# Kernel optimization log

Hardware: AMD Instinct MI355X
Metric: run time of the kernel (lower is better)

Reference implementation:

```python
import jax, jax.numpy as jnp
import numpy as np

PS = 16          # patch size == conv kernel == stride
EPS = 1e-5       # BatchNorm eps (torch default)


def setup_inputs() -> dict:
    key = jax.random.key(0)
    ks = jax.random.split(key, 12)
    B, Cin, H = 64, 3, 256
    D, Dm = 3, 768                      # private_depth, hidden_dim
    P = (H // PS) ** 2                  # num_patches = 256

    x = jax.random.normal(ks[0], (B, Cin, H, H), jnp.float32)
    # patch-embed conv: weight [O, I, kh, kw], bias [O]
    conv0_w = jax.random.normal(ks[1], (Dm, Cin, PS, PS), jnp.float32) * 0.02
    conv0_b = jax.random.normal(ks[2], (Dm,), jnp.float32) * 0.02
    # depth x (1x1 conv + BN): stacked params
    w1 = jax.random.normal(ks[3], (D, Dm, Dm), jnp.float32) * 0.02   # [O, I]
    b1 = jax.random.normal(ks[4], (D, Dm), jnp.float32) * 0.02
    gamma = jnp.ones((D, Dm), jnp.float32)
    beta = jnp.zeros((D, Dm), jnp.float32)
    # positional embedding [1, P, Dm]
    pos_emb = jax.random.normal(ks[5], (1, P, Dm), jnp.float32)
    # mixer Linear [out, in] + bias
    mixer_w = jax.random.normal(ks[6], (Dm, Dm), jnp.float32) * 0.02
    mixer_b = jax.random.normal(ks[7], (Dm,), jnp.float32) * 0.02
    # per-sample random permutation of the P patches (replaces randperm loop)
    perm = jax.vmap(lambda k: jax.random.permutation(k, P))(
        jax.random.split(ks[8], B)).astype(jnp.int32)

    return {"x": x, "conv0_w": conv0_w, "conv0_b": conv0_b, "w1": w1,
            "b1": b1, "gamma": gamma, "beta": beta, "pos_emb": pos_emb,
            "mixer_w": mixer_w, "mixer_b": mixer_b, "perm": perm}


def reference(x, conv0_w, conv0_b, w1, b1, gamma, beta, pos_emb,
              mixer_w, mixer_b, perm):
    B, Cin, H, W = x.shape
    hp, wp = H // PS, W // PS
    Dm = conv0_w.shape[0]

    # non-overlapping patch conv == reshape + matmul
    # x -> [B, hp*wp, Cin*PS*PS] with (c, kh, kw) flattening matching conv weight
    patches = x.reshape(B, Cin, hp, PS, wp, PS).transpose(0, 2, 4, 1, 3, 5)
    patches = patches.reshape(B, hp * wp, Cin * PS * PS)
    h = jax.nn.relu(patches @ conv0_w.reshape(Dm, -1).T + conv0_b)  # [B, P, Dm]

    # private_depth x (1x1 conv -> BN (batch stats, no running stats) -> ReLU)
    for d in range(w1.shape[0]):
        h = h @ w1[d].T + b1[d]
        mu = h.mean(axis=(0, 1))                      # per-channel over (B, H*W)
        var = ((h - mu) ** 2).mean(axis=(0, 1))       # biased variance
        h = (h - mu) * jax.lax.rsqrt(var + EPS) * gamma[d] + beta[d]
        h = jax.nn.relu(h)

    # pos embedding + mixer (ReLU -> Linear)
    h = h + pos_emb
    h = jax.nn.relu(h) @ mixer_w.T + mixer_b          # [B, P, Dm]

    # per-sample pixel shuffle: shuffled[i, j] = h[i, perm[i, j]]
    out = jnp.take_along_axis(h, perm[:, :, None].astype(jnp.int32), axis=1)
    return out
```

## Files before the change

kernel.cpp:

```cpp
#include <hip/hip_runtime.h>
#include <hip/hip_bf16.h>
#include <stdint.h>

#define M_TOT 16384
#define DM 768
#define BM 256
#define BN 192
#define NKT3 12
#define QOFF (128 * DM)

typedef __attribute__((ext_vector_type(4))) float f32x4;
typedef __attribute__((ext_vector_type(8))) short short8;
typedef __attribute__((ext_vector_type(8))) unsigned short ushort8;
typedef __attribute__((ext_vector_type(4))) unsigned short ushort4v;

__device__ __forceinline__ unsigned short f2bf(float f) {
    union { float f; unsigned u; } v; v.f = f;
    unsigned r = v.u + 0x7fffu + ((v.u >> 16) & 1u);
    return (unsigned short)(r >> 16);
}
__device__ __forceinline__ float bf2f(unsigned short h) {
    union { unsigned u; float f; } v; v.u = ((unsigned)h) << 16;
    return v.f;
}

__device__ __forceinline__ void gload_lds16(const unsigned short* g, unsigned short* l) {
    __builtin_amdgcn_global_load_lds(
        (const __attribute__((address_space(1))) void*)g,
        (__attribute__((address_space(3))) void*)l, 16, 0, 0);
}

__global__ __launch_bounds__(256)
void prep(const float* __restrict__ cw, const float* __restrict__ w1,
          const float* __restrict__ mw, const int* __restrict__ perm,
          unsigned short* __restrict__ wA, unsigned short* __restrict__ wD,
          unsigned short* __restrict__ wM, int* __restrict__ invp)
{
    int b = blockIdx.x;
    if (b < 2880) {
        int i = b * 256 + threadIdx.x;
        const float* src; unsigned short* dst; int off;
        if (i < 147456)              { src = cw; dst = wA; off = i; }
        else if (i < 147456+442368)  { src = w1; dst = wD; off = i - 147456; }
        else                         { src = mw; dst = wM; off = i - 589824; }
        f32x4 v = ((const f32x4*)src)[off];
        ushort4v o;
        o.x = f2bf(v.x); o.y = f2bf(v.y); o.z = f2bf(v.z); o.w = f2bf(v.w);
        ((ushort4v*)dst)[off] = o;
    } else {
        int i = (b - 2880) * 256 + threadIdx.x;
        int bb = i >> 8;
        invp[(bb << 8) + perm[i]] = i & 255;
    }
}

__global__ __launch_bounds__(256)
void im2col(const float* __restrict__ x, unsigned short* __restrict__ patches)
{
    int t = blockIdx.x * 256 + threadIdx.x;
    int bp = t / 192;
    int q  = t - bp * 192;
    int c   = q >> 6;
    int kh  = (q >> 2) & 15;
    int kw0 = (q & 3) << 2;
    int b = bp >> 8, p = bp & 255;
    int ph = p >> 4, pw = p & 15;
    const float* src = x + ((((size_t)b * 3 + c) * 256 + ph * 16 + kh) * 256 + pw * 16 + kw0);
    f32x4 v = *(const f32x4*)src;
    ushort4v o;
    o.x = f2bf(v.x); o.y = f2bf(v.y); o.z = f2bf(v.z); o.w = f2bf(v.w);
    *(ushort4v*)(patches + (size_t)bp * DM + (q << 2)) = o;
}

#define VM4  asm volatile("s_waitcnt vmcnt(4)" ::: "memory");
#define VM0  asm volatile("s_waitcnt vmcnt(0)" ::: "memory");
#define LGKM0 asm volatile("s_waitcnt lgkmcnt(0)" ::: "memory");
#define BARR asm volatile("s_barrier" ::: "memory");

#define PH(AB, BB, MH, KS, LOADB, PRE, POST)                                     \
  {                                                                              \
    if (LOADB) {                                                                 \
      _Pragma("unroll")                                                          \
      for (int j = 0; j < 3; ++j)                                                \
        breg[j] = *(const short8*)((const char*)Bb + (size_t)(BB) * (BN*64*2) +  \
                  (wc * 48 + j * 16 + frow) * 128 + (((KS) * 64 + fq16) ^ rswz));\
    }                                                                            \
    short8 af[4];                                                                \
    _Pragma("unroll")                                                            \
    for (int i = 0; i < 4; ++i)                                                  \
      af[i] = *(const short8*)((const char*)Aa + (size_t)(AB) * (BM*64*2) +      \
              (wr * 128 + (MH) * 64 + i * 16 + frow) * 128 +                     \
              (((KS) * 64 + fq16) ^ rswz));                                      \
    PRE;                                                                         \
    __builtin_amdgcn_s_setprio(1);                                               \
    _Pragma("unroll")                                                            \
    for (int i = 0; i < 4; ++i)                                                  \
      _Pragma("unroll")                                                          \
      for (int j = 0; j < 3; ++j)                                                \
        acc[(MH) * 4 + i][j] = __builtin_amdgcn_mfma_f32_16x16x32_bf16(          \
            af[i], breg[j], acc[(MH) * 4 + i][j], 0, 0, 0);                      \
    __builtin_amdgcn_s_setprio(0);                                               \
    POST;                                                                        \
    BARR                                                                         \
  }

template<int EPI, int BNA>
__global__ __launch_bounds__(512, 2)
void gemm8p(const unsigned short* __restrict__ A,
            const unsigned short* __restrict__ Bw,
            const float* __restrict__ bias,
            void* __restrict__ outp,
            const int* __restrict__ invp,
            float* __restrict__ bnpart,
            const float* __restrict__ ssA,
            const float* __restrict__ pos)
{
    __shared__ unsigned short Aa[3][BM * 64];
    __shared__ unsigned short Bb[2][BN * 64];

    const int tid  = threadIdx.x;
    const int w    = tid >> 6;
    const int lane = tid & 63;
    const int wr = w >> 2, wc = w & 3;

    int bid = blockIdx.x;
    int nb  = (bid & 7) * 32 + (bid >> 3);
    const int tileM = nb >> 2, tileN = nb & 3;
    const int m0 = tileM * BM, n0 = tileN * BN;

    const int sRow = lane >> 3;
    const int swzc = ((lane & 7) * 16) ^ ((sRow & 7) << 4);
    const unsigned short* gA0 = A  + (size_t)(m0 + w * 32 + sRow) * DM + (swzc >> 1);
    const unsigned short* gB0 = Bw + (size_t)(n0 + w * 24 + sRow) * DM + (swzc >> 1);

    auto STAGE_A = [&](int buf, int kt) {
        #pragma unroll
        for (int j = 0; j < 4; ++j)
            gload_lds16(gA0 + (size_t)j * 8 * DM + kt * 64,
                        &Aa[buf][(w * 32 + j * 8) * 64]);
    };
    auto STAGE_B = [&](int buf, int kt) {
        #pragma unroll
        for (int j = 0; j < 3; ++j)
            gload_lds16(gB0 + (size_t)j * 8 * DM + kt * 64,
                        &Bb[buf][(w * 24 + j * 8) * 64]);
    };

    const int rRow0 = w * 32 + (lane >> 3);
    const unsigned short* gAr = A + (size_t)(m0 + rRow0) * DM + (lane & 7) * 8;
    const int wrswz = (lane >> 3) << 4;
    ushort8 aldr[4];

    auto ALOAD = [&](int t) {
        #pragma unroll
        for (int j = 0; j < 4; ++j)
            aldr[j] = *(const ushort8*)(gAr + (size_t)j * 8 * DM + t * 64);
    };
    auto XFORM = [&](int t, int tb) {
        const int k0 = t * 64 + (lane & 7) * 8;
        f32x4 sa = *(const f32x4*)(ssA + k0);
        f32x4 sb = *(const f32x4*)(ssA + k0 + 4);
        f32x4 ha = *(const f32x4*)(ssA + DM + k0);
        f32x4 hb = *(const f32x4*)(ssA + DM + k0 + 4);
        #pragma unroll
        for (int j = 0; j < 4; ++j) {
            int row = rRow0 + j * 8;
            f32x4 pa, pb;
            if (BNA == 2) {
                pa = *(const f32x4*)(pos + row * DM + k0);
                pb = *(const f32x4*)(pos + row * DM + k0 + 4);
            }
            ushort8 u = aldr[j];
            ushort8 o;
            #pragma unroll
            for (int e = 0; e < 8; ++e) {
                float f = bf2f(u[e]);
                float sc = (e < 4) ? sa[e] : sb[e - 4];
                float sh = (e < 4) ? ha[e] : hb[e - 4];
                float y = fmaxf(fmaf(sc, f, sh), 0.0f);
                if (BNA == 2) {
                    float pv = (e < 4) ? pa[e] : pb[e - 4];
                    y = fmaxf(y + pv, 0.0f);
                }
                o[e] = f2bf(y);
            }
            *(ushort8*)((char*)Aa + (size_t)tb * (BM*64*2) + row * 128 +
                        (((lane & 7) * 16) ^ wrswz)) = o;
        }
    };

    const int frow = lane & 15;
    const int fq16 = (lane >> 4) * 16;
    const int rswz = (lane & 7) << 4;

    f32x4 acc[8][3] = {};
    short8 breg[3];

    if (BNA == 0) {
        STAGE_A(0, 0);
        STAGE_B(0, 0);
        STAGE_A(1, 1);
        VM4
        BARR
    } else {
        ALOAD(0); XFORM(0, 0);
        ALOAD(1); XFORM(1, 1);
        STAGE_B(0, 0);
        VM0
        LGKM0
        BARR
    }

    if (BNA == 0) {
        #pragma unroll
        for (int kt = 0; kt < NKT3; ++kt) {
            const int ab = kt % 3, bb = kt & 1;
            PH(ab, bb, 0, 0, 1, { if (kt < 11) STAGE_B((kt + 1) & 1, kt + 1); }, {})
            PH(ab, bb, 1, 0, 0, { if (kt < 10) STAGE_A((kt + 2) % 3, kt + 2); }, {})
            PH(ab, bb, 0, 1, 1, {}, {})
            if (kt < 10)       { PH(ab, bb, 1, 1, 0, {}, { VM4 }) }
            else if (kt == 10) { PH(ab, bb, 1, 1, 0, {}, { VM0 }) }
            else               { PH(ab, bb, 1, 1, 0, {}, {}) }
        }
    } else {
        #pragma unroll 3
        for (int kt = 0; kt < NKT3; ++kt) {
            const int ab = kt % 3, bb = kt & 1;
            const int ab1 = (ab == 2) ? 0 : ab + 1;
            PH(ab, bb, 0, 0, 1, { if (kt < 11) STAGE_B((kt + 1) & 1, kt + 1); }, {})
            PH(ab, bb, 1, 0, 0, { if (kt >= 1 && kt < 11) XFORM(kt + 1, ab1); },
                                { if (kt >= 1 && kt < 11) LGKM0 })
            PH(ab, bb, 0, 1, 1, {}, {})
            PH(ab, bb, 1, 1, 0, {}, { if (kt < 11) VM0
                                      if (kt < 10) ALOAD(kt + 2); })
        }
    }

    const int crow = (lane >> 4) * 4;
    const int ccol = lane & 15;
    const int nbase = n0 + wc * 48;

    float bv[3];
    #pragma unroll
    for (int j = 0; j < 3; ++j) bv[j] = bias[nbase + j * 16 + ccol];

    if (EPI == 0) {
        unsigned short* O = (unsigned short*)outp;
        #pragma unroll
        for (int mi = 0; mi < 8; ++mi) {
            #pragma unroll
            for (int r = 0; r < 4; ++r) {
                int m = m0 + wr * 128 + mi * 16 + crow + r;
                unsigned short* orow = O + (size_t)m * DM + nbase + ccol;
                #pragma unroll
                for (int j = 0; j < 3; ++j)
                    orow[j * 16] = f2bf(fmaxf(acc[mi][j][r] + bv[j], 0.0f));
            }
        }
    }

    if (EPI == 2) {
        float* O = (float*)outp;
        #pragma unroll
        for (int mi = 0; mi < 8; ++mi) {
            #pragma unroll
            for (int r = 0; r < 4; ++r) {
                int m = m0 + wr * 128 + mi * 16 + crow + r;
                int mo = (m & ~255) | invp[m];
                float* orow = O + (size_t)mo * DM + nbase + ccol;
                #pragma unroll
                for (int j = 0; j < 3; ++j)
                    orow[j * 16] = acc[mi][j][r] + bv[j];
            }
        }
    }

    if (EPI == 1) {
        unsigned short* O = (unsigned short*)outp;
        #pragma unroll
        for (int mi = 0; mi < 8; ++mi) {
            #pragma unroll
            for (int r = 0; r < 4; ++r) {
                int m = m0 + wr * 128 + mi * 16 + crow + r;
                unsigned short* orow = O + (size_t)m * DM + nbase + ccol;
                #pragma unroll
                for (int j = 0; j < 3; ++j)
                    orow[j * 16] = f2bf(acc[mi][j][r] + bv[j]);
            }
        }
        #pragma unroll
        for (int j = 0; j < 3; ++j) {
            float s = 0.f, q = 0.f;
            #pragma unroll
            for (int mi = 0; mi < 8; ++mi)
                #pragma unroll
                for (int r = 0; r < 4; ++r) {
                    float v = acc[mi][j][r] + bv[j];
                    s += v; q += v * v;
                }
            s += __shfl_xor(s, 16); s += __shfl_xor(s, 32);
            q += __shfl_xor(q, 16); q += __shfl_xor(q, 32);
            if (lane < 16) {
                int c  = nbase + j * 16 + lane;
                int ri = tileM * 2 + wr;
                bnpart[(size_t)c * 128 + ri]        = s;
                bnpart[QOFF + (size_t)c * 128 + ri] = q;
            }
        }
    }
}

__global__ void bn_stats(const float* __restrict__ part, const float* __restrict__ gamma,
                         const float* __restrict__ beta, float* __restrict__ ss)
{
    int c = blockIdx.x * 256 + threadIdx.x;
    const float* ps = part + (size_t)c * 128;
    const float* pq = part + QOFF + (size_t)c * 128;
    float s = 0.f, q = 0.f;
    #pragma unroll 8
    for (int i = 0; i < 128; ++i) { s += ps[i]; q += pq[i]; }
    float mu  = s * (1.0f / 16384.0f);
    float var = q * (1.0f / 16384.0f) - mu * mu;
    float scale = rsqrtf(var + 1e-5f) * gamma[c];
    ss[c] = scale;
    ss[DM + c] = beta[c] - mu * scale;
}

extern "C" void kernel_launch(void* const* d_in, const int* in_sizes, int n_in,
                              void* d_out, int out_size, void* d_ws, size_t ws_size,
                              hipStream_t stream)
{
    (void)in_sizes; (void)n_in; (void)out_size; (void)ws_size;

    const float* x       = (const float*)d_in[0];
    const float* conv0_w = (const float*)d_in[1];
    const float* conv0_b = (const float*)d_in[2];
    const float* w1      = (const float*)d_in[3];
    const float* b1      = (const float*)d_in[4];
    const float* gamma   = (const float*)d_in[5];
    const float* beta    = (const float*)d_in[6];
    const float* pos     = (const float*)d_in[7];
    const float* mixer_w = (const float*)d_in[8];
    const float* mixer_b = (const float*)d_in[9];
    const int*   perm    = (const int*)d_in[10];

    unsigned short* actA = (unsigned short*)d_ws;
    unsigned short* actB = actA + (size_t)M_TOT * DM;
    unsigned short* wA   = actB + (size_t)M_TOT * DM;
    unsigned short* wD   = wA + DM * DM;
    unsigned short* wM   = wD + 3 * DM * DM;
    float* bnpart = (float*)(wM + DM * DM);
    float* ss     = bnpart + 2 * 128 * DM;
    int*   invp   = (int*)(ss + 2 * DM);

    prep<<<2944, 256, 0, stream>>>(conv0_w, w1, mixer_w, perm, wA, wD, wM, invp);
    im2col<<<12288, 256, 0, stream>>>(x, actA);

    gemm8p<0, 0><<<256, 512, 0, stream>>>(actA, wA, conv0_b, actB, nullptr,
                                          nullptr, nullptr, nullptr);
    gemm8p<1, 0><<<256, 512, 0, stream>>>(actB, wD + 0 * (size_t)DM * DM, b1 + 0 * DM,
                                          actA, nullptr, bnpart, nullptr, nullptr);
    bn_stats<<<3, 256, 0, stream>>>(bnpart, gamma + 0 * DM, beta + 0 * DM, ss);
    gemm8p<1, 1><<<256, 512, 0, stream>>>(actA, wD + 1 * (size_t)DM * DM, b1 + 1 * DM,
                                          actB, nullptr, bnpart, ss, nullptr);
    bn_stats<<<3, 256, 0, stream>>>(bnpart, gamma + 1 * DM, beta + 1 * DM, ss);
    gemm8p<1, 1><<<256, 512, 0, stream>>>(actB, wD + 2 * (size_t)DM * DM, b1 + 2 * DM,
                                          actA, nullptr, bnpart, ss, nullptr);
    bn_stats<<<3, 256, 0, stream>>>(bnpart, gamma + 2 * DM, beta + 2 * DM, ss);
    gemm8p<2, 2><<<256, 512, 0, stream>>>(actA, wM, mixer_b, d_out, invp,
                                          nullptr, ss, pos);
}
```

Before: 212.0 us.

## Merge prep with im2col and split final BN+pos transform into standalone kernel

Folds the im2col conversion into the weight-prep kernel so one launch does both. It also moves the last BN scale/shift, ReLU and positional-embedding add out of the mixer GEMM's A-load path into a separate elementwise kernel, so the mixer GEMM uses the plain bf16 pipeline (BNA=0). This trades an extra launch plus a full bf16 activation read and write for a simpler GEMM main loop that no longer loads pos in fp32.

New measurement: 207.4 us. 2.1% less time.

```diff
diff --git a/kernel.cpp b/kernel.cpp
--- a/kernel.cpp
+++ b/kernel.cpp
@@ -31,14 +31,30 @@
 }
 
 __global__ __launch_bounds__(256)
-void prep(const float* __restrict__ cw, const float* __restrict__ w1,
-          const float* __restrict__ mw, const int* __restrict__ perm,
-          unsigned short* __restrict__ wA, unsigned short* __restrict__ wD,
-          unsigned short* __restrict__ wM, int* __restrict__ invp)
+void prepim(const float* __restrict__ cw, const float* __restrict__ w1,
+            const float* __restrict__ mw, const int* __restrict__ perm,
+            const float* __restrict__ x,
+            unsigned short* __restrict__ wA, unsigned short* __restrict__ wD,
+            unsigned short* __restrict__ wM, int* __restrict__ invp,
+            unsigned short* __restrict__ patches)
 {
     int b = blockIdx.x;
-    if (b < 2880) {
-        int i = b * 256 + threadIdx.x;
+    if (b < 12288) {
+        int t = b * 256 + threadIdx.x;
+        int bp = t / 192;
+        int q  = t - bp * 192;
+        int c   = q >> 6;
+        int kh  = (q >> 2) & 15;
+        int kw0 = (q & 3) << 2;
+        int bb = bp >> 8, p = bp & 255;
+        int ph = p >> 4, pw = p & 15;
+        const float* src = x + ((((size_t)bb * 3 + c) * 256 + ph * 16 + kh) * 256 + pw * 16 + kw0);
+        f32x4 v = *(const f32x4*)src;
+        ushort4v o;
+        o.x = f2bf(v.x); o.y = f2bf(v.y); o.z = f2bf(v.z); o.w = f2bf(v.w);
+        *(ushort4v*)(patches + (size_t)bp * DM + (q << 2)) = o;
+    } else if (b < 12288 + 2880) {
+        int i = (b - 12288) * 256 + threadIdx.x;
         const float* src; unsigned short* dst; int off;
         if (i < 147456)              { src = cw; dst = wA; off = i; }
         else if (i < 147456+442368)  { src = w1; dst = wD; off = i - 147456; }
@@ -48,28 +64,10 @@
         o.x = f2bf(v.x); o.y = f2bf(v.y); o.z = f2bf(v.z); o.w = f2bf(v.w);
         ((ushort4v*)dst)[off] = o;
     } else {
-        int i = (b - 2880) * 256 + threadIdx.x;
+        int i = (b - 12288 - 2880) * 256 + threadIdx.x;
         int bb = i >> 8;
         invp[(bb << 8) + perm[i]] = i & 255;
     }
-}
-
-__global__ __launch_bounds__(256)
-void im2col(const float* __restrict__ x, unsigned short* __restrict__ patches)
-{
-    int t = blockIdx.x * 256 + threadIdx.x;
-    int bp = t / 192;
-    int q  = t - bp * 192;
-    int c   = q >> 6;
-    int kh  = (q >> 2) & 15;
-    int kw0 = (q & 3) << 2;
-    int b = bp >> 8, p = bp & 255;
-    int ph = p >> 4, pw = p & 15;
-    const float* src = x + ((((size_t)b * 3 + c) * 256 + ph * 16 + kh) * 256 + pw * 16 + kw0);
-    f32x4 v = *(const f32x4*)src;
-    ushort4v o;
-    o.x = f2bf(v.x); o.y = f2bf(v.y); o.z = f2bf(v.z); o.w = f2bf(v.w);
-    *(ushort4v*)(patches + (size_t)bp * DM + (q << 2)) = o;
 }
 
 #define VM4  asm volatile("s_waitcnt vmcnt(4)" ::: "memory");
@@ -112,8 +110,7 @@
             void* __restrict__ outp,
             const int* __restrict__ invp,
             float* __restrict__ bnpart,
-            const float* __restrict__ ssA,
-            const float* __restrict__ pos)
+            const float* __restrict__ ssA)
 {
     __shared__ unsigned short Aa[3][BM * 64];
     __shared__ unsigned short Bb[2][BN * 64];
@@ -165,11 +162,6 @@
         #pragma unroll
         for (int j = 0; j < 4; ++j) {
             int row = rRow0 + j * 8;
-            f32x4 pa, pb;
-            if (BNA == 2) {
-                pa = *(const f32x4*)(pos + row * DM + k0);
-                pb = *(const f32x4*)(pos + row * DM + k0 + 4);
-            }
             ushort8 u = aldr[j];
             ushort8 o;
             #pragma unroll
@@ -177,12 +169,7 @@
                 float f = bf2f(u[e]);
                 float sc = (e < 4) ? sa[e] : sb[e - 4];
                 float sh = (e < 4) ? ha[e] : hb[e - 4];
-                float y = fmaxf(fmaf(sc, f, sh), 0.0f);
-                if (BNA == 2) {
-                    float pv = (e < 4) ? pa[e] : pb[e - 4];
-                    y = fmaxf(y + pv, 0.0f);
-                }
-                o[e] = f2bf(y);
+                o[e] = f2bf(fmaxf(fmaf(sc, f, sh), 0.0f));
             }
             *(ushort8*)((char*)Aa + (size_t)tb * (BM*64*2) + row * 128 +
                         (((lane & 7) * 16) ^ wrswz)) = o;
@@ -326,6 +313,34 @@
     ss[DM + c] = beta[c] - mu * scale;
 }
 
+__global__ __launch_bounds__(256)
+void bnpos_apply(const unsigned short* __restrict__ hin, const float* __restrict__ ss,
+                 const float* __restrict__ pos, unsigned short* __restrict__ hout)
+{
+    __shared__ float sc[DM], sh[DM];
+    const int t = threadIdx.x;
+    #pragma unroll
+    for (int i = 0; i < 3; ++i) {
+        sc[t + i * 256] = ss[t + i * 256];
+        sh[t + i * 256] = ss[DM + t + i * 256];
+    }
+    __syncthreads();
+
+    int g = blockIdx.x * 256 + t;
+    int row = g / 96;
+    int c0 = (g - row * 96) * 8;
+    const short8 v = *(const short8*)(hin + (size_t)row * DM + c0);
+    short8 o;
+    #pragma unroll
+    for (int e = 0; e < 8; ++e) {
+        float xv = bf2f((unsigned short)v[e]);
+        float y = fmaxf(xv * sc[c0 + e] + sh[c0 + e], 0.0f);
+        y = fmaxf(y + pos[(row & 255) * DM + c0 + e], 0.0f);
+        o[e] = (short)f2bf(y);
+    }
+    *(short8*)(hout + (size_t)row * DM + c0) = o;
+}
+
 extern "C" void kernel_launch(void* const* d_in, const int* in_sizes, int n_in,
                               void* d_out, int out_size, void* d_ws, size_t ws_size,
                               hipStream_t stream)
@@ -353,20 +368,21 @@
     float* ss     = bnpart + 2 * 128 * DM;
     int*   invp   = (int*)(ss + 2 * DM);
 
-    prep<<<2944, 256, 0, stream>>>(conv0_w, w1, mixer_w, perm, wA, wD, wM, invp);
-    im2col<<<12288, 256, 0, stream>>>(x, actA);
+    prepim<<<15232, 256, 0, stream>>>(conv0_w, w1, mixer_w, perm, x,
+                                      wA, wD, wM, invp, actA);
 
     gemm8p<0, 0><<<256, 512, 0, stream>>>(actA, wA, conv0_b, actB, nullptr,
-                                          nullptr, nullptr, nullptr);
+                                          nullptr, nullptr);
     gemm8p<1, 0><<<256, 512, 0, stream>>>(actB, wD + 0 * (size_t)DM * DM, b1 + 0 * DM,
-                                          actA, nullptr, bnpart, nullptr, nullptr);
+                                          actA, nullptr, bnpart, nullptr);
     bn_stats<<<3, 256, 0, stream>>>(bnpart, gamma + 0 * DM, beta + 0 * DM, ss);
     gemm8p<1, 1><<<256, 512, 0, stream>>>(actA, wD + 1 * (size_t)DM * DM, b1 + 1 * DM,
-                                          actB, nullptr, bnpart, ss, nullptr);
+                                          actB, nullptr, bnpart, ss);
     bn_stats<<<3, 256, 0, stream>>>(bnpart, gamma + 1 * DM, beta + 1 * DM, ss);
     gemm8p<1, 1><<<256, 512, 0, stream>>>(actB, wD + 2 * (size_t)DM * DM, b1 + 2 * DM,
-                                          actA, nullptr, bnpart, ss, nullptr);
+                                          actA, nullptr, bnpart, ss);
     bn_stats<<<3, 256, 0, stream>>>(bnpart, gamma + 2 * DM, beta + 2 * DM, ss);
-    gemm8p<2, 2><<<256, 512, 0, stream>>>(actA, wM, mixer_b, d_out, invp,
-                                          nullptr, ss, pos);
-}
+    bnpos_apply<<<6144, 256, 0, stream>>>(actA, ss, pos, actB);
+    gemm8p<2, 0><<<256, 512, 0, stream>>>(actB, wM, mixer_b, d_out, invp,
+                                          nullptr, nullptr);
+}
```
